# Optimization experiments

Hardware: AMD Instinct MI355X
Metric: run time of the kernel (lower is better)

The kernel has to match this reference:

```python
import jax, jax.numpy as jnp
import numpy as np

THRESH = 0.95
SCALE = 20.0
KERNEL = 8  # feature_hw // proto_grid_size = 64 // 8
EPS = 1e-4


def _avg_pool(x, k):
    # x: [b, c, h, w] -> [b, c, h//k, w//k], non-overlapping k x k mean (AvgPool2d(k))
    b, c, h, w = x.shape
    return x.reshape(b, c, h // k, k, w // k, k).mean(axis=(3, 5))


def _safe_norm(x, eps=EPS):
    # L2-normalize along axis 1, clamping the norm at eps (matches safe_norm)
    n = jnp.sqrt(jnp.sum(x * x, axis=1, keepdims=True))
    return x / jnp.maximum(n, eps)


def setup_inputs() -> dict:
    key = jax.random.key(0)
    k1, k2, k3 = jax.random.split(key, 3)
    qry = jax.random.normal(k1, (32, 256, 64, 64), dtype=jnp.float32)
    sup_x = jax.random.normal(k2, (4, 256, 64, 64), dtype=jnp.float32)
    # binary support mask so that (sup_y > 0.95) selects the ones and pooled
    # occupancy exceeds 0.5 for ~half the grid cells -> valid prototypes exist
    sup_y = jax.random.randint(k3, (4, 1, 64, 64), 0, 2).astype(jnp.float32)
    return {"qry": qry, "sup_x": sup_x, "sup_y": sup_y}


def reference(qry, sup_x, sup_y):
    # ---- normalize query features (gridconv mode) ----
    qn = _safe_norm(qry)                                  # [B, C, H, W]

    # ---- prototype extraction (gridconv) ----
    mask_bin = (sup_y > THRESH).astype(qry.dtype)         # [bs, 1, H, W]
    feat_pooled = _avg_pool(sup_x, KERNEL)                # [bs, C, G, G]
    mask_pooled = _avg_pool(mask_bin, KERNEL)             # [bs, 1, G, G]
    valid = (mask_pooled[:, 0] > 0.5).reshape(-1)         # [P] with P = bs*G*G

    C = feat_pooled.shape[1]
    # gather all pooled locations in (image, hi, wi) order, mask out invalid ones
    protos = jnp.transpose(feat_pooled, (0, 2, 3, 1)).reshape(-1, C)  # [P, C]
    protos_n = _safe_norm(protos)                         # [P, C]

    # ---- prediction: conv2d with 1x1 prototype kernels == channel contraction ----
    dists = jnp.einsum('bchw,pc->bphw', qn, protos_n) * SCALE  # [B, P, H, W]
    vmask = valid[None, :, None, None]
    logits = jnp.where(vmask, dists, -jnp.inf)
    w = jax.nn.softmax(logits, axis=1)                    # invalid protos get 0 weight
    pred = jnp.sum(w * jnp.where(vmask, dists, 0.0), axis=1, keepdims=True)  # [B,1,H,W]

    debug_assign = jnp.argmax(logits, axis=1).astype(dists.dtype)  # [B, H, W]
    proto_grid = mask_bin                                 # (sup_y > thresh).float()
    return (pred, debug_assign, proto_grid)
```

## Files before the change

### kernel.cpp

```cpp
#include <hip/hip_runtime.h>
#include <math.h>

constexpr int BQ = 32;
constexpr int C  = 256;
constexpr int HW = 4096;
constexpr int W  = 64;
constexpr int P  = 256;
constexpr float THRESH = 0.95f;
constexpr float SCALE  = 20.0f;
constexpr float EPSF   = 1e-4f;
constexpr double EPSD  = 1e-4;
constexpr float GAP_THRESH = 2e-3f;
constexpr int MAXSUS = 65536;

constexpr int OUT_ASSIGN = BQ * HW;
constexpr int OUT_GRID   = 2 * BQ * HW;

typedef __attribute__((ext_vector_type(8))) short short8;
typedef __attribute__((ext_vector_type(4))) float floatx4;

static __device__ __forceinline__ unsigned short f2bf(float x) {
    unsigned u = __float_as_uint(x);
    u += 0x7FFFu + ((u >> 16) & 1u);
    return (unsigned short)(u >> 16);
}
static __device__ __forceinline__ float bf2f(unsigned short h) {
    return __uint_as_float(((unsigned)h) << 16);
}

#define FRAGOFF(tile, ks, h, lane) (((((tile) * 8 + (ks)) * 2 + (h)) * 64 + (lane)) * 8)

static __device__ __forceinline__ void gl_lds16(const unsigned short* gp, unsigned short* lp) {
    __builtin_amdgcn_global_load_lds(
        (const __attribute__((address_space(1))) unsigned int*)gp,
        (__attribute__((address_space(3))) unsigned int*)lp, 16, 0, 0);
}

__global__ __launch_bounds__(256)
void prep_kernel(const float* __restrict__ sup_x, const float* __restrict__ sup_y,
                 float* __restrict__ out, unsigned short* __restrict__ pB,
                 double* __restrict__ pn64, int* __restrict__ valid,
                 int* __restrict__ counter)
{
    const int p = blockIdx.x;
    const int t = threadIdx.x;
    const int s = p >> 6, gy = (p >> 3) & 7, gx = p & 7;

    const float* base = sup_x + ((size_t)(s * C + t)) * HW + (gy * 8) * W + gx * 8;
    double sum = 0.0;
#pragma unroll
    for (int r = 0; r < 8; ++r) {
        const float4 a  = *(const float4*)(base + r * W);
        const float4 bq = *(const float4*)(base + r * W + 4);
        sum += (double)a.x;  sum += (double)a.y;  sum += (double)a.z;  sum += (double)a.w;
        sum += (double)bq.x; sum += (double)bq.y; sum += (double)bq.z; sum += (double)bq.w;
    }
    const double mean = sum * (1.0 / 64.0);

    __shared__ double red[256];
    red[t] = mean * mean;
    __syncthreads();
    for (int off = 128; off > 0; off >>= 1) {
        if (t < off) red[t] += red[t + off];
        __syncthreads();
    }
    const double nrm = sqrt(red[0]);
    const double pnv = mean / fmax(nrm, EPSD);
    pn64[(size_t)p * C + t] = pnv;

    const float pnf = (float)pnv;
    const unsigned short phi = f2bf(pnf);
    const unsigned short plo = f2bf(pnf - bf2f(phi));
    const int nt = p >> 4, ks = t >> 5, lane = (((t >> 3) & 3) << 4) | (p & 15), j = t & 7;
    pB[FRAGOFF(nt, ks, 0, lane) + j] = phi;
    pB[FRAGOFF(nt, ks, 1, lane) + j] = plo;

    bool mybit = false;
    if (t < 64) {
        const int r = t >> 3, k = t & 7;
        mybit = sup_y[s * HW + (gy * 8 + r) * W + gx * 8 + k] > THRESH;
    }
    const unsigned long long bm = __ballot(mybit);
    if (t == 0) {
        valid[p] = (__popcll(bm) > 32) ? 1 : 0;
        if (p == 0) *counter = 0;
    }
    if (t < 64) {
        const int i = p * 64 + t;
        out[OUT_GRID + i] = (sup_y[i] > THRESH) ? 1.0f : 0.0f;
    }
}

__global__ __launch_bounds__(256, 4)
void dist_kernel(const float* __restrict__ qry, const unsigned short* __restrict__ pB,
                 const int* __restrict__ valid, float* __restrict__ out,
                 int* __restrict__ counter, int* __restrict__ suspects)
{
    __shared__ unsigned short ldsB[16 * 2 * 64 * 8];
    __shared__ int validLds[P];

    const int t    = threadIdx.x;
    const int w    = t >> 6;
    const int l    = t & 63;
    const int quad = l >> 4;
    const int m    = l & 15;

    const int b    = blockIdx.x >> 6;
    const int pos0 = (blockIdx.x & 63) * 64;

    validLds[t] = valid[t];

    const float* qp = qry + (size_t)b * C * HW + pos0 + w * 16 + m;

    floatx4 acc[16];
#pragma unroll
    for (int nt = 0; nt < 16; ++nt) acc[nt] = (floatx4){0.f, 0.f, 0.f, 0.f};

    float vbuf[8];
#pragma unroll
    for (int j = 0; j < 8; ++j)
        vbuf[j] = qp[(size_t)(quad * 8 + j) * HW];

    float ssq = 0.f;
#pragma unroll
    for (int ks = 0; ks < 8; ++ks) {
        __syncthreads();
#pragma unroll
        for (int i = 0; i < 8; ++i) {
            const int idx = w * 8 + i, nt = idx >> 1, h = idx & 1;
            gl_lds16(pB + FRAGOFF(nt, ks, h, 0) + l * 8,
                     &ldsB[(nt * 2 + h) * 512]);
        }
        short8 h8, l8;
#pragma unroll
        for (int j = 0; j < 8; ++j) {
            const float v = vbuf[j];
            ssq = fmaf(v, v, ssq);
            const unsigned short hi = f2bf(v);
            h8[j] = (short)hi;
            l8[j] = (short)f2bf(v - bf2f(hi));
        }
        if (ks < 7) {
#pragma unroll
            for (int j = 0; j < 8; ++j)
                vbuf[j] = qp[(size_t)((ks + 1) * 32 + quad * 8 + j) * HW];
        }
        __syncthreads();
#pragma unroll
        for (int nt = 0; nt < 16; ++nt) {
            const short8 bh = *(const short8*)&ldsB[((nt * 2 + 0) * 64 + l) * 8];
            const short8 bl = *(const short8*)&ldsB[((nt * 2 + 1) * 64 + l) * 8];
            acc[nt] = __builtin_amdgcn_mfma_f32_16x16x32_bf16(h8, bh, acc[nt], 0, 0, 0);
            acc[nt] = __builtin_amdgcn_mfma_f32_16x16x32_bf16(h8, bl, acc[nt], 0, 0, 0);
            acc[nt] = __builtin_amdgcn_mfma_f32_16x16x32_bf16(l8, bh, acc[nt], 0, 0, 0);
        }
    }

    ssq += __shfl_xor(ssq, 16);
    ssq += __shfl_xor(ssq, 32);
    const float scalev = SCALE / fmaxf(sqrtf(ssq), EPSF);

    int vbits = 0;
#pragma unroll
    for (int nt = 0; nt < 16; ++nt) vbits |= validLds[nt * 16 + m] << nt;

    float scr[4];
#pragma unroll
    for (int r = 0; r < 4; ++r) scr[r] = __shfl(scalev, quad * 4 + r);
#pragma unroll
    for (int nt = 0; nt < 16; ++nt)
#pragma unroll
        for (int r = 0; r < 4; ++r) acc[nt][r] *= scr[r];

#pragma unroll
    for (int r = 0; r < 4; ++r) {
        float m1 = -INFINITY, m2 = -INFINITY; int id = 0x7fffffff;
#pragma unroll
        for (int nt = 0; nt < 16; ++nt) {
            if (vbits & (1 << nt)) {
                const float d = acc[nt][r];
                if (d > m1)      { m2 = m1; m1 = d; id = nt * 16 + m; }
                else if (d > m2) { m2 = d; }
            }
        }
#pragma unroll
        for (int sh = 1; sh < 16; sh <<= 1) {
            const float om1 = __shfl_xor(m1, sh);
            const float om2 = __shfl_xor(m2, sh);
            const int   oid = __shfl_xor(id, sh);
            if (om1 > m1) { m2 = fmaxf(m1, om2); m1 = om1; id = oid; }
            else { if (om1 == m1 && oid < id) id = oid; m2 = fmaxf(m2, om1); }
        }
        const int posg = b * HW + pos0 + w * 16 + quad * 4 + r;
        if (m == 0) {
            out[OUT_ASSIGN + posg] = (float)id;
            if (m1 - m2 < GAP_THRESH) {
                const int slot = atomicAdd(counter, 1);
                if (slot < MAXSUS) suspects[slot] = posg;
            }
        }
        float se = 0.f, sw = 0.f;
#pragma unroll
        for (int nt = 0; nt < 16; ++nt) {
            if (vbits & (1 << nt)) {
                const float d = acc[nt][r];
                const float e = __expf(d - m1);
                se += e; sw = fmaf(e, d, sw);
            }
        }
#pragma unroll
        for (int sh = 1; sh < 16; sh <<= 1) {
            se += __shfl_xor(se, sh);
            sw += __shfl_xor(sw, sh);
        }
        if (m == 0) out[posg] = sw / se;
    }
}

__global__ __launch_bounds__(256)
void recheck_kernel(const float* __restrict__ qry, const double* __restrict__ pn64,
                    const int* __restrict__ valid, const int* __restrict__ counter,
                    const int* __restrict__ suspects, float* __restrict__ out)
{
    __shared__ float qsh[4][256];
    const int t = threadIdx.x;
    const int w = t >> 6, l = t & 63;
    int n = *counter; if (n > MAXSUS) n = MAXSUS;
    const int nb = (n + 3) >> 2;

    for (int batch = blockIdx.x; batch < nb; batch += gridDim.x) {
        const int si = batch * 4 + w;
        const bool active = si < n;
        int pos = 0;
        if (active) {
            pos = suspects[si];
#pragma unroll
            for (int k = 0; k < 4; ++k) {
                const int c = l + 64 * k;
                qsh[w][c] = qry[(size_t)(pos >> 12) * (C * HW) + (size_t)c * HW + (pos & (HW - 1))];
            }
        }
        __syncthreads();
        if (active) {
            double best = -INFINITY; int bid = 0x7fffffff;
#pragma unroll
            for (int k = 0; k < 4; ++k) {
                const int p = l + 64 * k;
                if (valid[p]) {
                    const double* pr = pn64 + (size_t)p * C;
                    double a0 = 0.0, a1 = 0.0, a2 = 0.0, a3 = 0.0;
#pragma unroll 4
                    for (int c = 0; c < C; c += 4) {
                        a0 = fma((double)qsh[w][c + 0], pr[c + 0], a0);
                        a1 = fma((double)qsh[w][c + 1], pr[c + 1], a1);
                        a2 = fma((double)qsh[w][c + 2], pr[c + 2], a2);
                        a3 = fma((double)qsh[w][c + 3], pr[c + 3], a3);
                    }
                    const double d = (a0 + a1) + (a2 + a3);
                    if (d > best) { best = d; bid = p; }
                }
            }
#pragma unroll
            for (int sh = 1; sh < 64; sh <<= 1) {
                const double od = __shfl_xor(best, sh);
                const int    oi = __shfl_xor(bid, sh);
                if (od > best || (od == best && oi < bid)) { best = od; bid = oi; }
            }
            if (l == 0) out[OUT_ASSIGN + pos] = (float)bid;
        }
        __syncthreads();
    }
}

extern "C" void kernel_launch(void* const* d_in, const int* in_sizes, int n_in,
                              void* d_out, int out_size, void* d_ws, size_t ws_size,
                              hipStream_t stream)
{
    const float* qry   = (const float*)d_in[0];
    const float* sup_x = (const float*)d_in[1];
    const float* sup_y = (const float*)d_in[2];
    float* out = (float*)d_out;
    char*  ws  = (char*)d_ws;

    unsigned short* pB       = (unsigned short*)(ws);
    double*         pn64     = (double*)(ws + 256 * 1024);
    int*            valid    = (int*)(ws + 768 * 1024);
    int*            counter  = (int*)(ws + 768 * 1024 + 1024);
    int*            suspects = (int*)(ws + 768 * 1024 + 2048);

    prep_kernel<<<dim3(P), dim3(256), 0, stream>>>(sup_x, sup_y, out, pB, pn64, valid, counter);
    dist_kernel<<<dim3(BQ * (HW / 64)), dim3(256), 0, stream>>>(qry, pB, valid, out, counter, suspects);
    recheck_kernel<<<dim3(1024), dim3(256), 0, stream>>>(qry, pn64, valid, counter, suspects, out);
}
```

Before: 274.7 us.

## Double-buffer prototype fragments in LDS with half-size phases

Splits each K-step into two phases of 8 prototype tiles and double-buffers the LDS prototype staging. The next phase's global-to-LDS copy is issued before the MFMAs on the current buffer, so the copy can overlap compute, and each phase needs only one barrier instead of two. LDS use per block stays the same. The cost is twice as many phases and barriers in total, plus extra control logic around the query conversion.

```diff
diff --git a/kernel.cpp b/kernel.cpp
--- a/kernel.cpp
+++ b/kernel.cpp
@@ -96,7 +96,7 @@
                  const int* __restrict__ valid, float* __restrict__ out,
                  int* __restrict__ counter, int* __restrict__ suspects)
 {
-    __shared__ unsigned short ldsB[16 * 2 * 64 * 8];
+    __shared__ unsigned short ldsB[2][8 * 2 * 64 * 8];
     __shared__ int validLds[P];
 
     const int t    = threadIdx.x;
@@ -120,40 +120,56 @@
 #pragma unroll
     for (int j = 0; j < 8; ++j)
         vbuf[j] = qp[(size_t)(quad * 8 + j) * HW];
+#pragma unroll
+    for (int i = 0; i < 4; ++i) {
+        const int c = w * 4 + i, ntl = c >> 1, h = c & 1;
+        gl_lds16(pB + FRAGOFF(ntl, 0, h, 0) + l * 8,
+                 &ldsB[0][(ntl * 2 + h) * 512]);
+    }
+    __syncthreads();
 
     float ssq = 0.f;
-#pragma unroll
-    for (int ks = 0; ks < 8; ++ks) {
-        __syncthreads();
-#pragma unroll
-        for (int i = 0; i < 8; ++i) {
-            const int idx = w * 8 + i, nt = idx >> 1, h = idx & 1;
-            gl_lds16(pB + FRAGOFF(nt, ks, h, 0) + l * 8,
-                     &ldsB[(nt * 2 + h) * 512]);
-        }
-        short8 h8, l8;
-#pragma unroll
-        for (int j = 0; j < 8; ++j) {
-            const float v = vbuf[j];
-            ssq = fmaf(v, v, ssq);
-            const unsigned short hi = f2bf(v);
-            h8[j] = (short)hi;
-            l8[j] = (short)f2bf(v - bf2f(hi));
-        }
-        if (ks < 7) {
-#pragma unroll
-            for (int j = 0; j < 8; ++j)
-                vbuf[j] = qp[(size_t)((ks + 1) * 32 + quad * 8 + j) * HW];
-        }
-        __syncthreads();
-#pragma unroll
-        for (int nt = 0; nt < 16; ++nt) {
-            const short8 bh = *(const short8*)&ldsB[((nt * 2 + 0) * 64 + l) * 8];
-            const short8 bl = *(const short8*)&ldsB[((nt * 2 + 1) * 64 + l) * 8];
+    short8 h8, l8;
+#pragma unroll
+    for (int ph = 0; ph < 16; ++ph) {
+        const int ks   = ph >> 1;
+        const int half = ph & 1;
+        const int par  = ph & 1;
+
+        if (ph < 15) {
+            const int ks2 = (ph + 1) >> 1, half2 = (ph + 1) & 1;
+#pragma unroll
+            for (int i = 0; i < 4; ++i) {
+                const int c = w * 4 + i, ntl = c >> 1, h = c & 1;
+                gl_lds16(pB + FRAGOFF(half2 * 8 + ntl, ks2, h, 0) + l * 8,
+                         &ldsB[(ph + 1) & 1][(ntl * 2 + h) * 512]);
+            }
+        }
+        if (half == 0) {
+#pragma unroll
+            for (int j = 0; j < 8; ++j) {
+                const float v = vbuf[j];
+                ssq = fmaf(v, v, ssq);
+                const unsigned short hi = f2bf(v);
+                h8[j] = (short)hi;
+                l8[j] = (short)f2bf(v - bf2f(hi));
+            }
+            if (ks < 7) {
+#pragma unroll
+                for (int j = 0; j < 8; ++j)
+                    vbuf[j] = qp[(size_t)((ks + 1) * 32 + quad * 8 + j) * HW];
+            }
+        }
+#pragma unroll
+        for (int ntl = 0; ntl < 8; ++ntl) {
+            const short8 bh = *(const short8*)&ldsB[par][((ntl * 2 + 0) * 64 + l) * 8];
+            const short8 bl = *(const short8*)&ldsB[par][((ntl * 2 + 1) * 64 + l) * 8];
+            const int nt = half * 8 + ntl;
             acc[nt] = __builtin_amdgcn_mfma_f32_16x16x32_bf16(h8, bh, acc[nt], 0, 0, 0);
             acc[nt] = __builtin_amdgcn_mfma_f32_16x16x32_bf16(h8, bl, acc[nt], 0, 0, 0);
             acc[nt] = __builtin_amdgcn_mfma_f32_16x16x32_bf16(l8, bh, acc[nt], 0, 0, 0);
         }
+        __syncthreads();
     }
 
     ssq += __shfl_xor(ssq, 16);
```

New measurement: 457.1 us. 1.66x slower.
